# Performance work log

Measured on AMD Instinct MI355X. Metric: run time of the kernel, lower is better.

Reference implementation:

```python
import jax, jax.numpy as jnp
import numpy as np

VOCAB = 32000
DIM = 1024
DEPTH = 4
SEQ = 512
HEADS = 16
NMB = 4
MAXMEM = NMB * SEQ  # 2048
RAMP = 128
COEF = 1e-06
B = 4
DH = DIM // HEADS


def _ln(x, g, b):
    mu = jnp.mean(x, axis=-1, keepdims=True)
    v = jnp.mean((x - mu) ** 2, axis=-1, keepdims=True)
    return (x - mu) / jnp.sqrt(v + 1e-5) * g + b


def setup_inputs() -> dict:
    key = jax.random.key(0)
    ks = jax.random.split(key, 24)
    s = 0.02
    inp = {
        'tokens': jax.random.randint(ks[0], (B, SEQ), 0, VOCAB),
        'mems': jax.random.normal(ks[1], (DEPTH, B, MAXMEM, DIM), jnp.float32) * s,
        'times': jax.random.randint(ks[2], (DEPTH, MAXMEM), 0, 4096, dtype=jnp.int32),
        'token_emb': jax.random.normal(ks[3], (VOCAB, DIM), jnp.float32) * s,
        'expire_W': jax.random.normal(ks[4], (DEPTH, DIM), jnp.float32) * s,
        'expire_b': jnp.full((DEPTH,), -float(MAXMEM), jnp.float32),  # torch init constant
        'ln1_g': jnp.ones((DEPTH, DIM), jnp.float32),
        'ln1_b': jnp.zeros((DEPTH, DIM), jnp.float32),
        'Wq': jax.random.normal(ks[5], (DEPTH, DIM, DIM), jnp.float32) * s,
        'Wkv': jax.random.normal(ks[6], (DEPTH, DIM, 2 * DIM), jnp.float32) * s,
        'Wo': jax.random.normal(ks[7], (DEPTH, DIM, DIM), jnp.float32) * s,
        'bo': jnp.zeros((DEPTH, DIM), jnp.float32),
        'ln2_g': jnp.ones((DEPTH, DIM), jnp.float32),
        'ln2_b': jnp.zeros((DEPTH, DIM), jnp.float32),
        'W1': jax.random.normal(ks[8], (DEPTH, DIM, 4 * DIM), jnp.float32) * s,
        'b1': jnp.zeros((DEPTH, 4 * DIM), jnp.float32),
        'W2': jax.random.normal(ks[9], (DEPTH, 4 * DIM, DIM), jnp.float32) * s,
        'b2': jnp.zeros((DEPTH, DIM), jnp.float32),
        'logits_W': jax.random.normal(ks[10], (DIM, VOCAB), jnp.float32) * s,
        'logits_b': jnp.zeros((VOCAB,), jnp.float32),
    }
    return inp


def reference(tokens, mems, times, token_emb, expire_W, expire_b, ln1_g, ln1_b,
              Wq, Wkv, Wo, bo, ln2_g, ln2_b, W1, b1, W2, b2, logits_W, logits_b):
    n, M = SEQ, MAXMEM
    scale = DH ** -0.5
    x = token_emb[tokens]  # (B, n, DIM)
    # causal mask over concat(mem, x): query i may attend key j iff j <= i + M
    causal = jnp.triu(jnp.ones((n, M + n), bool), k=M + 1)  # True = masked
    aux = jnp.float32(0.0)
    new_mems, new_times = [], []
    tnew = jnp.arange(n - 1, -1, -1, dtype=times.dtype)
    for d in range(DEPTH):
        mem = mems[d]                       # (B, M, DIM)
        t = times[d].astype(jnp.float32)    # (M,)
        hidden = x
        # --- expire span: per-memory-slot soft retention mask ---
        exps = jax.nn.sigmoid(mem @ expire_W[d] + expire_b[d]) * M  # (B, M)
        r = exps[:, None, None, :] - t[None, None, None, :]          # (B,1,1,M)
        r = jnp.pad(r, ((0, 0), (0, 0), (0, 0), (0, n)), constant_values=1.0)
        emask = jnp.clip(r / RAMP + 1.0, 0.0, 1.0)                   # (B,1,1,M+n)
        # --- pre-norm causal attention over concat(mem, x_normed) ---
        xn = _ln(x, ln1_g[d], ln1_b[d])
        q = (xn @ Wq[d]).reshape(B, n, HEADS, DH).transpose(0, 2, 1, 3)
        ctx = jnp.concatenate([mem, xn], axis=1)                     # (B, M+n, DIM)
        kv = ctx @ Wkv[d]
        k = kv[..., :DIM].reshape(B, M + n, HEADS, DH).transpose(0, 2, 1, 3)
        v = kv[..., DIM:].reshape(B, M + n, HEADS, DH).transpose(0, 2, 1, 3)
        dots = jnp.einsum('bhid,bhjd->bhij', q, k) * scale
        dots = jnp.where(causal, -jnp.inf, dots)
        attn = jax.nn.softmax(dots, axis=-1) * emask
        out = jnp.einsum('bhij,bhjd->bhid', attn, v)
        out = out.transpose(0, 2, 1, 3).reshape(B, n, DIM)
        x = out @ Wo[d] + bo[d] + x
        # --- pre-norm FFN ---
        xn2 = _ln(x, ln2_g[d], ln2_b[d])
        x = jax.nn.gelu(xn2 @ W1[d] + b1[d], approximate=False) @ W2[d] + b2[d] + x
        aux = aux + (exps / SEQ).sum() * COEF
        # --- memory bookkeeping (detached) ---
        new_mems.append(jax.lax.stop_gradient(
            jnp.concatenate([mem, hidden], axis=1)[:, -M:]))
        new_times.append(jnp.concatenate([times[d] + n, tnew])[-M:])
    logits = x @ logits_W + logits_b
    return (logits, jnp.stack(new_mems), jnp.stack(new_times), aux)
```

## Files before the change

kernel.cpp:

```cpp
#include <hip/hip_runtime.h>
#include <cmath>

#define DIMC   1024
#define SEQC   512
#define BC     4
#define MC     2048
#define CTXC   2560
#define HEADSC 16
#define DHC    64
#define VOCABC 32000
#define MAXC   512

using short8 = __attribute__((ext_vector_type(8))) short;
using f32x4  = __attribute__((ext_vector_type(4))) float;
using u16x4  = __attribute__((ext_vector_type(4))) unsigned short;
using u16x8  = __attribute__((ext_vector_type(8))) unsigned short;

__device__ __forceinline__ unsigned short f2bf(float f) {
    unsigned u = __float_as_uint(f);
    unsigned r = (u + 0x7fffu + ((u >> 16) & 1u)) >> 16;
    return (unsigned short)r;
}

__device__ __forceinline__ void glds16(const unsigned short* g, char* l) {
    __builtin_amdgcn_global_load_lds(
        (const __attribute__((address_space(1))) void*)g,
        (__attribute__((address_space(3))) void*)l, 16, 0, 0);
}

__global__ __launch_bounds__(256) void embed_kernel(const int* __restrict__ tokens,
                                                    const float* __restrict__ emb,
                                                    float* __restrict__ x) {
    int row = blockIdx.x;
    int tok = tokens[row];
    const float4 v = *(const float4*)(emb + (size_t)tok * DIMC + threadIdx.x * 4);
    *(float4*)(x + (size_t)row * DIMC + threadIdx.x * 4) = v;
}

__global__ __launch_bounds__(256) void times_init_kernel(const int* __restrict__ times,
                                                         float* __restrict__ out_times,
                                                         float* __restrict__ aux) {
    int i = blockIdx.x * 256 + threadIdx.x;
    if (i == 0) aux[0] = 0.0f;
    if (i < 4 * MC) {
        int d = i >> 11, m = i & (MC - 1);
        out_times[i] = (m < MC - SEQC) ? (float)(times[d * MC + SEQC + m] + SEQC)
                                       : (float)(MC - 1 - m);
    }
}

#define PREP_MEM 8192
#define PREP_XC  10240
#define PREP_LN  12288
#define PREP_TOT 24576
__global__ __launch_bounds__(256) void prep_kernel(
    const float* __restrict__ mem_d, const float* __restrict__ x,
    const float* __restrict__ eW, const float* __restrict__ eb,
    float* __restrict__ exps, float* __restrict__ aux,
    unsigned short* __restrict__ mem_b, float* __restrict__ out_mems_d,
    const float* __restrict__ g1, const float* __restrict__ b1v,
    unsigned short* __restrict__ xn_b,
    const float* __restrict__ Wq, const float* __restrict__ Wkv,
    const float* __restrict__ Wo, const float* __restrict__ W1,
    const float* __restrict__ W2,
    unsigned short* __restrict__ wq_t, unsigned short* __restrict__ wkv_t,
    unsigned short* __restrict__ wo_t, unsigned short* __restrict__ w1_t,
    unsigned short* __restrict__ w2_t) {
    __shared__ float sh[1056];
    const int bid = blockIdx.x, tid = threadIdx.x;
    if (bid < PREP_MEM) {
        int row = bid;
        int m = row & 2047, b = row >> 11;
        const float4 v = *(const float4*)(mem_d + (size_t)row * DIMC + tid * 4);
        const float4 w = *(const float4*)(eW + tid * 4);
        float s = v.x * w.x + v.y * w.y + v.z * w.z + v.w * w.w;
        for (int off = 32; off; off >>= 1) s += __shfl_down(s, off, 64);
        int wid = tid >> 6, lane = tid & 63;
        if (lane == 0) sh[wid] = s;
        u16x4 o = { f2bf(v.x), f2bf(v.y), f2bf(v.z), f2bf(v.w) };
        *(u16x4*)(mem_b + (size_t)row * DIMC + tid * 4) = o;
        if (m >= SEQC)
            *(float4*)(out_mems_d + ((size_t)(b * MC + m - SEQC)) * DIMC + tid * 4) = v;
        __syncthreads();
        if (tid == 0) {
            float z = sh[0] + sh[1] + sh[2] + sh[3] + eb[0];
            float e = (float)MC / (1.0f + expf(-z));
            exps[row] = e;
            atomicAdd(aux, e * (1e-6f / (float)SEQC));
        }
    } else if (bid < PREP_XC) {
        int r = bid - PREP_MEM;
        int b = r >> 9, i = r & 511;
        const float4 v = *(const float4*)(x + (size_t)r * DIMC + tid * 4);
        *(float4*)(out_mems_d + ((size_t)(b * MC + MC - SEQC + i)) * DIMC + tid * 4) = v;
    } else if (bid < PREP_LN) {
        int row = bid - PREP_XC;
        const float4 v = *(const float4*)(x + (size_t)row * DIMC + tid * 4);
        float s = v.x + v.y + v.z + v.w;
        float q = v.x * v.x + v.y * v.y + v.z * v.z + v.w * v.w;
        for (int off = 32; off; off >>= 1) {
            s += __shfl_down(s, off, 64);
            q += __shfl_down(q, off, 64);
        }
        int wid = tid >> 6, lane = tid & 63;
        if (lane == 0) { sh[wid] = s; sh[4 + wid] = q; }
        __syncthreads();
        if (tid == 0) {
            float S = sh[0] + sh[1] + sh[2] + sh[3];
            float Q = sh[4] + sh[5] + sh[6] + sh[7];
            float mu = S / DIMC;
            float var = Q / DIMC - mu * mu;
            sh[8] = mu;
            sh[9] = rsqrtf(var + 1e-5f);
        }
        __syncthreads();
        float mu = sh[8], rstd = sh[9];
        const float4 gg = *(const float4*)(g1 + tid * 4);
        const float4 bb = *(const float4*)(b1v + tid * 4);
        u16x4 o = { f2bf((v.x - mu) * rstd * gg.x + bb.x),
                    f2bf((v.y - mu) * rstd * gg.y + bb.y),
                    f2bf((v.z - mu) * rstd * gg.z + bb.z),
                    f2bf((v.w - mu) * rstd * gg.w + bb.w) };
        *(u16x4*)(xn_b + (size_t)row * DIMC + tid * 4) = o;
    } else {
        int t = bid - PREP_LN;
        const float* W; unsigned short* Wt; int K, N, tx, ty;
        if (t < 1024)      { W = Wq;  Wt = wq_t;  K = 1024; N = 1024; tx = t & 31;  ty = t >> 5; }
        else if (t < 3072) { int u = t - 1024; W = Wkv; Wt = wkv_t; K = 1024; N = 2048; tx = u & 63;  ty = u >> 6; }
        else if (t < 4096) { int u = t - 3072; W = Wo;  Wt = wo_t;  K = 1024; N = 1024; tx = u & 31;  ty = u >> 5; }
        else if (t < 8192) { int u = t - 4096; W = W1;  Wt = w1_t;  K = 1024; N = 4096; tx = u & 127; ty = u >> 7; }
        else               { int u = t - 8192; W = W2;  Wt = w2_t;  K = 4096; N = 1024; tx = u & 31;  ty = u >> 5; }
        int n0 = tx * 32, k0 = ty * 32;
        int r = tid >> 3, c = (tid & 7) * 4;
        const float4 v = *(const float4*)(W + (size_t)(k0 + r) * N + n0 + c);
        sh[r * 33 + c] = v.x; sh[r * 33 + c + 1] = v.y;
        sh[r * 33 + c + 2] = v.z; sh[r * 33 + c + 3] = v.w;
        __syncthreads();
        u16x4 o = { f2bf(sh[(c + 0) * 33 + r]), f2bf(sh[(c + 1) * 33 + r]),
                    f2bf(sh[(c + 2) * 33 + r]), f2bf(sh[(c + 3) * 33 + r]) };
        *(u16x4*)(Wt + (size_t)(n0 + r) * K + k0 + c) = o;
    }
}

__global__ __launch_bounds__(64) void compact_kernel(
    const float* __restrict__ exps, const int* __restrict__ times_d,
    int* __restrict__ cidx, float* __restrict__ em_c, int* __restrict__ cnt) {
    int b = blockIdx.x, lane = threadIdx.x;
    int c = 0;
    for (int it = 0; it < 32; ++it) {
        int j = it * 64 + lane;
        float e = exps[b * MC + j];
        float rr = (e - (float)times_d[j]) * (1.0f / 128.0f) + 1.0f;
        float em = fminf(fmaxf(rr, 0.0f), 1.0f);
        unsigned long long mk = __ballot(em > 0.0f);
        int pos = c + __popcll(mk & ((1ull << lane) - 1ull));
        if (em > 0.0f) {
            cidx[b * 2048 + pos] = j;
            em_c[b * 2048 + pos] = em;
        }
        c += __popcll(mk);
    }
    int padded = (c + 63) & ~63;
    int fill_to = padded < MAXC ? MAXC : padded;
    for (int p = c + lane; p < fill_to; p += 64) {
        cidx[b * 2048 + p] = 0;
        em_c[b * 2048 + p] = 0.0f;
    }
    int tiles = padded >> 6;
    if (tiles > (MAXC >> 6)) tiles = MAXC >> 6;
    if (lane == 0) cnt[b] = tiles;
}

__global__ __launch_bounds__(256) void ln_kernel(const float* __restrict__ in,
                                                 const float* __restrict__ g,
                                                 const float* __restrict__ b,
                                                 unsigned short* __restrict__ outb) {
    int row = blockIdx.x;
    int tid = threadIdx.x;
    const float4 v = *(const float4*)(in + (size_t)row * DIMC + tid * 4);
    float s = v.x + v.y + v.z + v.w;
    float q = v.x * v.x + v.y * v.y + v.z * v.z + v.w * v.w;
    for (int off = 32; off; off >>= 1) {
        s += __shfl_down(s, off, 64);
        q += __shfl_down(q, off, 64);
    }
    __shared__ float ss[4], sq[4];
    int wid = tid >> 6, lane = tid & 63;
    if (lane == 0) { ss[wid] = s; sq[wid] = q; }
    __syncthreads();
    if (tid == 0) {
        float S = ss[0] + ss[1] + ss[2] + ss[3];
        float Q = sq[0] + sq[1] + sq[2] + sq[3];
        float mu = S / DIMC;
        float var = Q / DIMC - mu * mu;
        ss[0] = mu;
        sq[0] = rsqrtf(var + 1e-5f);
    }
    __syncthreads();
    float mu = ss[0], rstd = sq[0];
    const float4 gg = *(const float4*)(g + tid * 4);
    const float4 bb = *(const float4*)(b + tid * 4);
    u16x4 o = { f2bf((v.x - mu) * rstd * gg.x + bb.x),
                f2bf((v.y - mu) * rstd * gg.y + bb.y),
                f2bf((v.z - mu) * rstd * gg.z + bb.z),
                f2bf((v.w - mu) * rstd * gg.w + bb.w) };
    *(u16x4*)(outb + (size_t)row * DIMC + tid * 4) = o;
}

__global__ __launch_bounds__(256) void wt_kernel(const float* __restrict__ W,
                                                 unsigned short* __restrict__ Wt,
                                                 int K, int N) {
    __shared__ float t[32][33];
    int tid = threadIdx.x;
    int n0 = blockIdx.x * 32, k0 = blockIdx.y * 32;
    int r = tid >> 3, c = (tid & 7) * 4;
    const float4 v = *(const float4*)(W + (size_t)(k0 + r) * N + n0 + c);
    t[r][c] = v.x; t[r][c + 1] = v.y; t[r][c + 2] = v.z; t[r][c + 3] = v.w;
    __syncthreads();
    u16x4 o = { f2bf(t[c + 0][r]), f2bf(t[c + 1][r]),
                f2bf(t[c + 2][r]), f2bf(t[c + 3][r]) };
    *(u16x4*)(Wt + (size_t)(n0 + r) * K + k0 + c) = o;
}

template<int AMODE, bool BIAS, bool GELU, bool RES, int OMODE, int RT>
__device__ __forceinline__ void gemm_body(
    unsigned short* As, unsigned short* Bs,
    const unsigned short* __restrict__ A, const int* __restrict__ gidx,
    const unsigned short* __restrict__ Wt, const float* __restrict__ bias,
    const float* __restrict__ res, float* __restrict__ Cf,
    unsigned short* __restrict__ Cb, int K, int N, int bx, int by) {
    constexpr int MF = RT / 32;
    const int tid = threadIdx.x;
    const int lane = tid & 63, wave = tid >> 6;
    const int row0 = by * RT, col0 = bx * 128;

    const int seg = tid & 3;
    const int rr0 = tid >> 2;
    const unsigned short* arow[RT / 64];
    #pragma unroll
    for (int p = 0; p < RT / 64; ++p) {
        int r = row0 + p * 64 + rr0;
        if (AMODE == 2) {
            int b = r >> 9, slot = r & (MAXC - 1);
            arow[p] = A + ((size_t)(b * 2048 + gidx[b * 2048 + slot])) * K;
        } else {
            arow[p] = A + (size_t)r * K;
        }
        arow[p] += seg * 8;
    }
    const unsigned short* brow[2];
    #pragma unroll
    for (int p = 0; p < 2; ++p)
        brow[p] = Wt + (size_t)(col0 + p * 64 + rr0) * K + seg * 8;

    char* lA = (char*)As + (tid & 192) * 16;
    char* lB = (char*)Bs + (tid & 192) * 16;

    auto stage = [&](int k0, int q) {
        char* a = lA + q * (RT * 64);
        glds16(arow[0] + k0, a);
        if (RT == 128) glds16(arow[1] + k0, a + 4096);
        char* bp = lB + q * 8192;
        glds16(brow[0] + k0, bp);
        glds16(brow[1] + k0, bp + 4096);
    };

    f32x4 acc[MF][4] = {};

    const int wr = (wave >> 1) * (RT / 2), wc = (wave & 1) * 64;
    const int fr = lane & 15;
    const int k8 = (lane >> 4) * 8;

    stage(0, 0);
    int cur = 0;
    for (int k0 = 0; k0 < K; k0 += 32) {
        if (k0 + 32 < K) {
            stage(k0 + 32, cur ^ 1);
            if (RT == 128) asm volatile("s_waitcnt vmcnt(4)" ::: "memory");
            else           asm volatile("s_waitcnt vmcnt(3)" ::: "memory");
        } else {
            asm volatile("s_waitcnt vmcnt(0)" ::: "memory");
        }
        __builtin_amdgcn_s_barrier();
        __builtin_amdgcn_sched_barrier(0);
        const unsigned short* Ar = As + cur * (RT * 32) + (size_t)(wr + fr) * 32 + k8;
        const unsigned short* Br = Bs + cur * (128 * 32) + (size_t)(wc + fr) * 32 + k8;
        short8 a[MF], b[4];
        #pragma unroll
        for (int m = 0; m < MF; ++m) a[m] = *(const short8*)(Ar + m * 16 * 32);
        #pragma unroll
        for (int n = 0; n < 4; ++n) b[n] = *(const short8*)(Br + n * 16 * 32);
        #pragma unroll
        for (int m = 0; m < MF; ++m)
            #pragma unroll
            for (int n = 0; n < 4; ++n)
                acc[m][n] = __builtin_amdgcn_mfma_f32_16x16x32_bf16(a[m], b[n], acc[m][n], 0, 0, 0);
        __builtin_amdgcn_s_barrier();
        cur ^= 1;
    }

    const int orow = row0 + wr + (lane >> 4) * 4;
    const int ocol = col0 + wc + fr;
    if (OMODE >= 3) {
        #pragma unroll
        for (int n = 0; n < 4; ++n) {
            int c = ocol + n * 16;
            #pragma unroll
            for (int m = 0; m < MF; ++m) {
                int r0 = orow + m * 16;
                int b = r0 >> 9, i = r0 & 511;
                size_t addr = (OMODE == 3)
                    ? ((size_t)(b * 1024 + c)) * 512 + i
                    : ((size_t)(b * 1024 + c)) * MAXC + i;
                u16x4 o = { f2bf(acc[m][n][0]), f2bf(acc[m][n][1]),
                            f2bf(acc[m][n][2]), f2bf(acc[m][n][3]) };
                *(u16x4*)(Cb + addr) = o;
            }
        }
        return;
    }
    #pragma unroll
    for (int n = 0; n < 4; ++n) {
        int c = ocol + n * 16;
        float bv = BIAS ? bias[c] : 0.0f;
        #pragma unroll
        for (int m = 0; m < MF; ++m) {
            #pragma unroll
            for (int i = 0; i < 4; ++i) {
                int r0 = orow + m * 16 + i;
                size_t orr = r0;
                if (OMODE == 1) orr = (size_t)r0 + (size_t)(r0 >> 11) * 512;
                if (OMODE == 2) orr = (size_t)r0 + (size_t)(r0 >> 9) * 2048 + 2048;
                size_t idx = orr * N + c;
                float v = acc[m][n][i] + bv;
                if (GELU) v = 0.5f * v * (1.0f + erff(v * 0.70710678118f));
                if (RES) v += res[idx];
                if (Cf) Cf[idx] = v;
                if (Cb) Cb[idx] = f2bf(v);
            }
        }
    }
}

__global__ __launch_bounds__(256) void qkv_gemm_kernel(
    const unsigned short* __restrict__ xn_b, const unsigned short* __restrict__ mem_b,
    const unsigned short* __restrict__ wq_t, const unsigned short* __restrict__ wkv_t,
    const int* __restrict__ cidx, const int* __restrict__ cnt,
    unsigned short* __restrict__ qb, unsigned short* __restrict__ kvb,
    unsigned short* __restrict__ vTl, unsigned short* __restrict__ vTc) {
    __shared__ unsigned short As[2 * 128 * 32];
    __shared__ unsigned short Bs[2 * 128 * 32];
    int id = blockIdx.x;
    if (id < 128) {
        gemm_body<0, false, false, false, 0, 128>(As, Bs, xn_b, nullptr, wq_t,
            nullptr, nullptr, nullptr, qb, 1024, 1024, id & 7, id >> 3);
    } else if (id < 256) {
        id -= 128;
        gemm_body<0, false, false, false, 2, 128>(As, Bs, xn_b, nullptr, wkv_t,
            nullptr, nullptr, nullptr, kvb, 1024, 1024, id & 7, id >> 3);
    } else if (id < 768) {
        id -= 256;
        gemm_body<0, false, false, false, 1, 128>(As, Bs, mem_b, nullptr, wkv_t,
            nullptr, nullptr, nullptr, kvb, 1024, 1024, id & 7, id >> 3);
    } else if (id < 896) {
        id -= 768;
        gemm_body<0, false, false, false, 3, 128>(As, Bs, xn_b, nullptr,
            wkv_t + (size_t)1024 * 1024, nullptr, nullptr, nullptr, vTl,
            1024, 1024, id & 7, id >> 3);
    } else {
        id -= 896;
        int by = id >> 3;
        int b = (by * 64) >> 9, slot0 = (by * 64) & (MAXC - 1);
        if (slot0 >= cnt[b] * 64) return;
        gemm_body<2, false, false, false, 4, 64>(As, Bs, mem_b, cidx,
            wkv_t + (size_t)1024 * 1024, nullptr, nullptr, nullptr, vTc,
            1024, 1024, id & 7, by);
    }
}

__global__ __launch_bounds__(256) void gemm64_kernel(
    const unsigned short* __restrict__ A, const unsigned short* __restrict__ Wt,
    const float* __restrict__ bias, const float* __restrict__ res,
    float* __restrict__ Cf, unsigned short* __restrict__ Cb, int K) {
    __shared__ unsigned short As[2 * 64 * 32];
    __shared__ unsigned short Bs[2 * 128 * 32];
    gemm_body<0, true, false, true, 0, 64>(As, Bs, A, nullptr, Wt, bias, res,
        Cf, Cb, K, 1024, blockIdx.x, blockIdx.y);
}

__global__ __launch_bounds__(256) void ffn1_kernel(
    const unsigned short* __restrict__ A, const unsigned short* __restrict__ Wt,
    const float* __restrict__ bias, unsigned short* __restrict__ Cb) {
    __shared__ unsigned short As[2 * 128 * 32];
    __shared__ unsigned short Bs[2 * 128 * 32];
    gemm_body<0, true, true, false, 0, 128>(As, Bs, A, nullptr, Wt, bias, nullptr,
        nullptr, Cb, 1024, 4096, blockIdx.x, blockIdx.y);
}

__global__ __launch_bounds__(256) void logits_kernel(
    const unsigned short* __restrict__ A, const unsigned short* __restrict__ Wt,
    const float* __restrict__ bias, float* __restrict__ Cf) {
    __shared__ unsigned short As[2 * 128 * 32];
    __shared__ unsigned short Bs[2 * 128 * 32];
    int D = blockIdx.y * 16 + blockIdx.x;
    int wid = (D & 7) * 500 + (D >> 3);
    gemm_body<0, true, false, false, 0, 128>(As, Bs, A, nullptr, Wt, bias, nullptr,
        Cf, nullptr, 1024, VOCABC, wid >> 4, wid & 15);
}

__global__ __launch_bounds__(512) void attn_mfma_kernel(
    const unsigned short* __restrict__ qb,
    const unsigned short* __restrict__ kvb,
    const unsigned short* __restrict__ vTl,
    const unsigned short* __restrict__ vTc,
    const int* __restrict__ cidx,
    const float* __restrict__ em_c,
    const int* __restrict__ cnt,
    unsigned short* __restrict__ outb) {
    __shared__ unsigned short K_s[2][64 * 64];
    __shared__ unsigned short V_s[2][64 * 64];
    __shared__ unsigned short p_s[8][16][72];
    __shared__ float em_s[64];
    const int tid = threadIdx.x;
    const int lane = tid & 63, wave = tid >> 6;
    const int qt = blockIdx.x, h = blockIdx.y, b = blockIdx.z;
    const int fr = lane & 15, g = lane >> 4;
    const int gq = qt * 128 + wave * 16;

    short8 aq[2];
    {
        const unsigned short* qp = qb + ((size_t)(b * SEQC + gq + fr)) * DIMC + h * DHC + g * 8;
        aq[0] = *(const short8*)qp;
        aq[1] = *(const short8*)(qp + 32);
    }

    const int sr = tid >> 3, ss = tid & 7;
    const int sw = (ss ^ (sr & 7)) * 8;
    const int wbase = (tid & 448) * 16;

    f32x4 acc_o[4] = {};
    float m_q = -1e30f, l_q = 0.0f;

    const int nlt = 2 * (qt + 1);
    const int nt = 32 + nlt;

    auto stage12 = [&](int t, int q) {
        const int jbase = t * 64;
        glds16(kvb + ((size_t)(b * CTXC + jbase + sr)) * 1024 + h * DHC + sw,
               (char*)K_s[q] + wbase);
        if (t >= 32)
            glds16(vTl + ((size_t)(b * 1024 + h * DHC + sr)) * 512 + (jbase - 2048) + sw,
                   (char*)V_s[q] + wbase);
    };

    stage12(0, 0);
    asm volatile("s_waitcnt vmcnt(0)" ::: "memory");
    __builtin_amdgcn_s_barrier();
    int cur = 0;
    for (int t = 0; t < nt; ++t) {
        if (t + 1 < nt) stage12(t + 1, cur ^ 1);
        if (t + 1 >= nt)      asm volatile("s_waitcnt vmcnt(0)" ::: "memory");
        else if (t >= 31)     asm volatile("s_waitcnt vmcnt(2)" ::: "memory");
        else                  asm volatile("s_waitcnt vmcnt(1)" ::: "memory");
        __builtin_amdgcn_s_barrier();
        __builtin_amdgcn_sched_barrier(0);

        const bool live = (t < 32) || ((t - 32) * 64 <= gq + 15);
        if (live) {
            f32x4 sT[4] = {};
            #pragma unroll
            for (int ks = 0; ks < 2; ++ks)
                #pragma unroll
                for (int mf = 0; mf < 4; ++mf) {
                    int row = mf * 16 + fr, sg = (ks * 4 + g) ^ (row & 7);
                    short8 kk = *(const short8*)((const char*)K_s[cur] + row * 128 + sg * 16);
                    sT[mf] = __builtin_amdgcn_mfma_f32_16x16x32_bf16(kk, aq[ks], sT[mf], 0, 0, 0);
                }

            if (t < 32) {
                float mx = sT[0][0];
                #pragma unroll
                for (int mf = 0; mf < 4; ++mf)
                    #pragma unroll
                    for (int i = 0; i < 4; ++i) mx = fmaxf(mx, sT[mf][i]);
                mx *= 0.125f;
                mx = fmaxf(mx, __shfl_xor(mx, 16, 64));
                mx = fmaxf(mx, __shfl_xor(mx, 32, 64));
                float mnew = fmaxf(m_q, mx);
                float fs = __expf(m_q - mnew);
                m_q = mnew;
                float ps = 0.0f;
                #pragma unroll
                for (int mf = 0; mf < 4; ++mf)
                    #pragma unroll
                    for (int i = 0; i < 4; ++i)
                        ps += __expf(sT[mf][i] * 0.125f - mnew);
                ps += __shfl_xor(ps, 16, 64);
                ps += __shfl_xor(ps, 32, 64);
                l_q = l_q * fs + ps;
            } else {
                const int lt = t - 32;
                const int kq = gq + fr - lt * 64;
                float sv[4][4];
                #pragma unroll
                for (int mf = 0; mf < 4; ++mf)
                    #pragma unroll
                    for (int i = 0; i < 4; ++i) {
                        int kl = mf * 16 + g * 4 + i;
                        sv[mf][i] = (kl <= kq) ? sT[mf][i] * 0.125f : -1e30f;
                    }
                float mx = sv[0][0];
                #pragma unroll
                for (int mf = 0; mf < 4; ++mf)
                    #pragma unroll
                    for (int i = 0; i < 4; ++i) mx = fmaxf(mx, sv[mf][i]);
                mx = fmaxf(mx, __shfl_xor(mx, 16, 64));
                mx = fmaxf(mx, __shfl_xor(mx, 32, 64));
                float mnew = fmaxf(m_q, mx);
                float fs = __expf(m_q - mnew);
                m_q = mnew;
                float ps = 0.0f;
                #pragma unroll
                for (int mf = 0; mf < 4; ++mf)
                    #pragma unroll
                    for (int i = 0; i < 4; ++i) {
                        float pe = __expf(sv[mf][i] - mnew);
                        ps += pe;
                        p_s[wave][fr][mf * 16 + g * 4 + i] = f2bf(pe);
                    }
                ps += __shfl_xor(ps, 16, 64);
                ps += __shfl_xor(ps, 32, 64);
                l_q = l_q * fs + ps;
                float fsr[4];
                #pragma unroll
                for (int i = 0; i < 4; ++i) fsr[i] = __shfl(fs, g * 4 + i, 64);
                #pragma unroll
                for (int n = 0; n < 4; ++n)
                    #pragma unroll
                    for (int i = 0; i < 4; ++i) acc_o[n][i] *= fsr[i];
                asm volatile("s_waitcnt lgkmcnt(0)" ::: "memory");
                #pragma unroll
                for (int ks = 0; ks < 2; ++ks) {
                    short8 ap = *(const short8*)&p_s[wave][fr][ks * 32 + g * 8];
                    #pragma unroll
                    for (int n = 0; n < 4; ++n) {
                        int row = n * 16 + fr, sg = (ks * 4 + g) ^ (row & 7);
                        short8 bv = *(const short8*)((const char*)V_s[cur] + row * 128 + sg * 16);
                        acc_o[n] = __builtin_amdgcn_mfma_f32_16x16x32_bf16(ap, bv, acc_o[n], 0, 0, 0);
                    }
                }
            }
        }
        __builtin_amdgcn_s_barrier();
        cur ^= 1;
    }

    const int nct = cnt[b];
    for (int ct = 0; ct < nct; ++ct) {
        __syncthreads();
        {
            int row = cidx[b * 2048 + ct * 64 + sr];
            glds16(kvb + ((size_t)(b * CTXC + row)) * 1024 + h * DHC + sw,
                   (char*)K_s[0] + wbase);
            glds16(vTc + ((size_t)(b * 1024 + h * DHC + sr)) * MAXC + ct * 64 + sw,
                   (char*)V_s[0] + wbase);
        }
        if (tid < 64) em_s[tid] = em_c[b * 2048 + ct * 64 + tid];
        __syncthreads();
        f32x4 sT[4] = {};
        #pragma unroll
        for (int ks = 0; ks < 2; ++ks)
            #pragma unroll
            for (int mf = 0; mf < 4; ++mf) {
                int row = mf * 16 + fr, sg = (ks * 4 + g) ^ (row & 7);
                short8 kk = *(const short8*)((const char*)K_s[0] + row * 128 + sg * 16);
                sT[mf] = __builtin_amdgcn_mfma_f32_16x16x32_bf16(kk, aq[ks], sT[mf], 0, 0, 0);
            }
        #pragma unroll
        for (int mf = 0; mf < 4; ++mf)
            #pragma unroll
            for (int i = 0; i < 4; ++i) {
                int key = mf * 16 + g * 4 + i;
                float pe = __expf(sT[mf][i] * 0.125f - m_q) * em_s[key];
                p_s[wave][fr][key] = f2bf(pe);
            }
        asm volatile("s_waitcnt lgkmcnt(0)" ::: "memory");
        #pragma unroll
        for (int ks = 0; ks < 2; ++ks) {
            short8 ap = *(const short8*)&p_s[wave][fr][ks * 32 + g * 8];
            #pragma unroll
            for (int n = 0; n < 4; ++n) {
                int row = n * 16 + fr, sg = (ks * 4 + g) ^ (row & 7);
                short8 bv = *(const short8*)((const char*)V_s[0] + row * 128 + sg * 16);
                acc_o[n] = __builtin_amdgcn_mfma_f32_16x16x32_bf16(ap, bv, acc_o[n], 0, 0, 0);
            }
        }
    }

    float linv = 1.0f / l_q;
    float invr[4];
    #pragma unroll
    for (int i = 0; i < 4; ++i) invr[i] = __shfl(linv, g * 4 + i, 64);
    #pragma unroll
    for (int n = 0; n < 4; ++n) {
        #pragma unroll
        for (int i = 0; i < 4; ++i) {
            size_t idx = ((size_t)(b * SEQC + gq + g * 4 + i)) * DIMC + h * DHC + n * 16 + fr;
            outb[idx] = f2bf(acc_o[n][i] * invr[i]);
        }
    }
}

__global__ void aux_write_kernel(const float* __restrict__ aux, float* __restrict__ dst) {
    dst[0] = aux[0];
}

extern "C" void kernel_launch(void* const* d_in, const int* in_sizes, int n_in,
                              void* d_out, int out_size, void* d_ws, size_t ws_size,
                              hipStream_t stream) {
    const int*   tokens    = (const int*)d_in[0];
    const float* mems      = (const float*)d_in[1];
    const int*   times     = (const int*)d_in[2];
    const float* token_emb = (const float*)d_in[3];
    const float* expire_W  = (const float*)d_in[4];
    const float* expire_b  = (const float*)d_in[5];
    const float* ln1_g     = (const float*)d_in[6];
    const float* ln1_b     = (const float*)d_in[7];
    const float* Wq        = (const float*)d_in[8];
    const float* Wkv       = (const float*)d_in[9];
    const float* Wo        = (const float*)d_in[10];
    const float* bo        = (const float*)d_in[11];
    const float* ln2_g     = (const float*)d_in[12];
    const float* ln2_b     = (const float*)d_in[13];
    const float* W1        = (const float*)d_in[14];
    const float* b1        = (const float*)d_in[15];
    const float* W2        = (const float*)d_in[16];
    const float* b2        = (const float*)d_in[17];
    const float* logits_W  = (const float*)d_in[18];
    const float* logits_b  = (const float*)d_in[19];

    float* out = (float*)d_out;
    float* ws  = (float*)d_ws;

    float* x = ws;
    unsigned short* qb_b  = (unsigned short*)(ws + 2097152);
    unsigned short* kv_b  = (unsigned short*)(ws + 3145728);
    unsigned short* vTl   = (unsigned short*)(ws + 8388608);
    unsigned short* vTc   = (unsigned short*)(ws + 9437184);
    unsigned short* xn_b  = (unsigned short*)(ws + 10485760);
    unsigned short* attn_b= (unsigned short*)(ws + 11534336);
    unsigned short* ffn_b = (unsigned short*)(ws + 12582912);
    unsigned short* mem_b = (unsigned short*)(ws + 16777216);
    unsigned short* x_b   = (unsigned short*)(ws + 20971520);
    unsigned short* wq_t  = (unsigned short*)(ws + 22020096);
    unsigned short* wkv_t = (unsigned short*)(ws + 22544384);
    unsigned short* wo_t  = (unsigned short*)(ws + 23592960);
    unsigned short* w1_t  = (unsigned short*)(ws + 24117248);
    unsigned short* w2_t  = (unsigned short*)(ws + 26214400);
    float* exps = ws + 28311552;
    float* aux  = ws + 28319744;
    int*   cidx = (int*)(ws + 28319760);
    float* em_c = ws + 28327952;
    int*   cnt  = (int*)(ws + 28336144);
    unsigned short* lw_t = (unsigned short*)(ws + 2097152);

    float* out_logits = out;
    float* out_mems   = out + 65536000;
    float* out_times  = out + 99090432;

    embed_kernel<<<BC * SEQC, 256, 0, stream>>>(tokens, token_emb, x);
    times_init_kernel<<<32, 256, 0, stream>>>(times, out_times, aux);

    for (int d = 0; d < 4; ++d) {
        const float* mem_d = mems + (size_t)d * BC * MC * DIMC;
        prep_kernel<<<PREP_TOT, 256, 0, stream>>>(
            mem_d, x, expire_W + d * DIMC, expire_b + d, exps, aux,
            mem_b, out_mems + (size_t)d * BC * MC * DIMC,
            ln1_g + d * DIMC, ln1_b + d * DIMC, xn_b,
            Wq + (size_t)d * DIMC * DIMC, Wkv + (size_t)d * DIMC * 2 * DIMC,
            Wo + (size_t)d * DIMC * DIMC, W1 + (size_t)d * DIMC * 4 * DIMC,
            W2 + (size_t)d * 4 * DIMC * DIMC,
            wq_t, wkv_t, wo_t, w1_t, w2_t);
        compact_kernel<<<BC, 64, 0, stream>>>(exps, times + d * MC, cidx, em_c, cnt);
        qkv_gemm_kernel<<<1152, 256, 0, stream>>>(xn_b, mem_b, wq_t, wkv_t,
                                                  cidx, cnt, qb_b, kv_b, vTl, vTc);
        attn_mfma_kernel<<<dim3(4, HEADSC, BC), 512, 0, stream>>>(
            qb_b, kv_b, vTl, vTc, cidx, em_c, cnt, attn_b);
        gemm64_kernel<<<dim3(8, 32), 256, 0, stream>>>(
            attn_b, wo_t, bo + d * DIMC, x, x, nullptr, DIMC);
        ln_kernel<<<BC * SEQC, 256, 0, stream>>>(x, ln2_g + d * DIMC, ln2_b + d * DIMC, xn_b);
        ffn1_kernel<<<dim3(32, 16), 256, 0, stream>>>(xn_b, w1_t, b1 + d * 4 * DIMC, ffn_b);
        if (d < 3) {
            gemm64_kernel<<<dim3(8, 32), 256, 0, stream>>>(
                ffn_b, w2_t, b2 + d * DIMC, x, x, nullptr, 4 * DIMC);
        } else {
            gemm64_kernel<<<dim3(8, 32), 256, 0, stream>>>(
                ffn_b, w2_t, b2 + d * DIMC, x, nullptr, x_b, 4 * DIMC);
        }
    }

    wt_kernel<<<dim3(1000, 32), 256, 0, stream>>>(logits_W, lw_t, DIMC, VOCABC);
    logits_kernel<<<dim3(16, 250), 256, 0, stream>>>(x_b, lw_t, logits_b, out_logits);
    aux_write_kernel<<<1, 1, 0, stream>>>(aux, out + 99098624);
}
```

Measured before the change: 1.731 ms.

## Use 256x256 tiles for logits GEMM and remap attention grid for XCD locality

```diff
diff --git a/kernel.cpp b/kernel.cpp
--- a/kernel.cpp
+++ b/kernel.cpp
@@ -397,15 +397,84 @@
         nullptr, Cb, 1024, 4096, blockIdx.x, blockIdx.y);
 }
 
-__global__ __launch_bounds__(256) void logits_kernel(
+__global__ __launch_bounds__(512, 2) void logits_kernel(
     const unsigned short* __restrict__ A, const unsigned short* __restrict__ Wt,
     const float* __restrict__ bias, float* __restrict__ Cf) {
-    __shared__ unsigned short As[2 * 128 * 32];
-    __shared__ unsigned short Bs[2 * 128 * 32];
-    int D = blockIdx.y * 16 + blockIdx.x;
-    int wid = (D & 7) * 500 + (D >> 3);
-    gemm_body<0, true, false, false, 0, 128>(As, Bs, A, nullptr, Wt, bias, nullptr,
-        Cf, nullptr, 1024, VOCABC, wid >> 4, wid & 15);
+    __shared__ unsigned short As[2 * 256 * 32];
+    __shared__ unsigned short Bs[2 * 256 * 32];
+    const int L = blockIdx.x;
+    const int wid = (L & 7) * 125 + (L >> 3);
+    const int ct = wid / 8, rt = wid & 7;
+    const int row0 = rt * 256, col0 = ct * 256;
+    const int tid = threadIdx.x;
+    const int lane = tid & 63, wave = tid >> 6;
+
+    const int seg = tid & 3;
+    const int rr0 = tid >> 2;
+    const unsigned short* arow[2];
+    const unsigned short* brow[2];
+    #pragma unroll
+    for (int p = 0; p < 2; ++p) {
+        arow[p] = A + (size_t)(row0 + p * 128 + rr0) * 1024 + seg * 8;
+        brow[p] = Wt + (size_t)(col0 + p * 128 + rr0) * 1024 + seg * 8;
+    }
+    char* lA = (char*)As + (tid & 448) * 16;
+    char* lB = (char*)Bs + (tid & 448) * 16;
+
+    auto stage = [&](int k0, int q) {
+        char* a = lA + q * 16384;
+        char* bp = lB + q * 16384;
+        glds16(arow[0] + k0, a);
+        glds16(arow[1] + k0, a + 8192);
+        glds16(brow[0] + k0, bp);
+        glds16(brow[1] + k0, bp + 8192);
+    };
+
+    f32x4 acc[8][4] = {};
+    const int wr = (wave >> 2) * 128, wc = (wave & 3) * 64;
+    const int fr = lane & 15;
+    const int k8 = (lane >> 4) * 8;
+
+    stage(0, 0);
+    int cur = 0;
+    for (int k0 = 0; k0 < 1024; k0 += 32) {
+        if (k0 + 32 < 1024) {
+            stage(k0 + 32, cur ^ 1);
+            asm volatile("s_waitcnt vmcnt(4)" ::: "memory");
+        } else {
+            asm volatile("s_waitcnt vmcnt(0)" ::: "memory");
+        }
+        __builtin_amdgcn_s_barrier();
+        __builtin_amdgcn_sched_barrier(0);
+        const unsigned short* Ar = As + cur * 8192 + (size_t)(wr + fr) * 32 + k8;
+        const unsigned short* Br = Bs + cur * 8192 + (size_t)(wc + fr) * 32 + k8;
+        short8 a[8], b[4];
+        #pragma unroll
+        for (int m = 0; m < 8; ++m) a[m] = *(const short8*)(Ar + m * 16 * 32);
+        #pragma unroll
+        for (int n = 0; n < 4; ++n) b[n] = *(const short8*)(Br + n * 16 * 32);
+        #pragma unroll
+        for (int m = 0; m < 8; ++m)
+            #pragma unroll
+            for (int n = 0; n < 4; ++n)
+                acc[m][n] = __builtin_amdgcn_mfma_f32_16x16x32_bf16(a[m], b[n], acc[m][n], 0, 0, 0);
+        __builtin_amdgcn_s_barrier();
+        cur ^= 1;
+    }
+
+    const int orow = row0 + wr + (lane >> 4) * 4;
+    const int ocol = col0 + wc + fr;
+    #pragma unroll
+    for (int n = 0; n < 4; ++n) {
+        int c = ocol + n * 16;
+        float bv = bias[c];
+        #pragma unroll
+        for (int m = 0; m < 8; ++m) {
+            #pragma unroll
+            for (int i = 0; i < 4; ++i)
+                Cf[(size_t)(orow + m * 16 + i) * VOCABC + c] = acc[m][n][i] + bv;
+        }
+    }
 }
 
 __global__ __launch_bounds__(512) void attn_mfma_kernel(
@@ -423,7 +492,11 @@
     __shared__ float em_s[64];
     const int tid = threadIdx.x;
     const int lane = tid & 63, wave = tid >> 6;
-    const int qt = blockIdx.x, h = blockIdx.y, b = blockIdx.z;
+    const int L = blockIdx.x;
+    const int ix = L >> 3;
+    const int qt = ix & 3;
+    const int gidx = (L & 7) * 8 + (ix >> 2);
+    const int h = gidx & 15, b = gidx >> 4;
     const int fr = lane & 15, g = lane >> 4;
     const int gq = qt * 128 + wave * 16;
 
@@ -684,7 +757,7 @@
         compact_kernel<<<BC, 64, 0, stream>>>(exps, times + d * MC, cidx, em_c, cnt);
         qkv_gemm_kernel<<<1152, 256, 0, stream>>>(xn_b, mem_b, wq_t, wkv_t,
                                                   cidx, cnt, qb_b, kv_b, vTl, vTc);
-        attn_mfma_kernel<<<dim3(4, HEADSC, BC), 512, 0, stream>>>(
+        attn_mfma_kernel<<<256, 512, 0, stream>>>(
             qb_b, kv_b, vTl, vTc, cidx, em_c, cnt, attn_b);
         gemm64_kernel<<<dim3(8, 32), 256, 0, stream>>>(
             attn_b, wo_t, bo + d * DIMC, x, x, nullptr, DIMC);
@@ -700,6 +773,6 @@
     }
 
     wt_kernel<<<dim3(1000, 32), 256, 0, stream>>>(logits_W, lw_t, DIMC, VOCABC);
-    logits_kernel<<<dim3(16, 250), 256, 0, stream>>>(x_b, lw_t, logits_b, out_logits);
+    logits_kernel<<<1000, 512, 0, stream>>>(x_b, lw_t, logits_b, out_logits);
     aux_write_kernel<<<1, 1, 0, stream>>>(aux, out + 99098624);
 }
```

New measurement: 1.727 ms. About the same (-0.2%).
